# Optimization experiments

Measured on AMD Instinct MI355X. Metric: run time of the kernel, lower is better.

## Reference

```python
import jax, jax.numpy as jnp
import numpy as np

EMBED_DIM = 1024
N_HEADS = 16
HEAD_DIM = EMBED_DIM // N_HEADS


def setup_inputs() -> dict:
    key = jax.random.key(0)
    k1, k2, k3 = jax.random.split(key, 3)
    B, T, D = 2, 2048, EMBED_DIM
    x = jax.random.normal(k1, (B, T, D), dtype=jnp.float32)
    # torch nn.Linear weights: (out_features, in_features); y = x @ W.T
    scale = 1.0 / np.sqrt(D)
    qkv_w = jax.random.uniform(k2, (3 * D, D), dtype=jnp.float32, minval=-scale, maxval=scale)
    out_w = jax.random.uniform(k3, (D, D), dtype=jnp.float32, minval=-scale, maxval=scale)
    return {"x": x, "qkv_w": qkv_w, "out_w": out_w}


def reference(x, qkv_w, out_w):
    B, T, D = x.shape
    H, hd = N_HEADS, HEAD_DIM
    qkv = jnp.einsum('btd,ed->bte', x, qkv_w)  # (B,T,3D)
    qkv = qkv.reshape(B, T, 3, H, hd)
    q = jnp.transpose(qkv[:, :, 0], (0, 2, 1, 3))  # (B,H,T,hd)
    k = jnp.transpose(qkv[:, :, 1], (0, 2, 1, 3))
    v = jnp.transpose(qkv[:, :, 2], (0, 2, 1, 3))
    scores = jnp.einsum('bhtd,bhsd->bhts', q, k) / np.sqrt(hd).astype(np.float32)
    causal = jnp.tril(jnp.ones((T, T), dtype=bool))  # True = keep
    scores = jnp.where(causal[None, None], scores, -jnp.inf)
    probs = jax.nn.softmax(scores, axis=-1)
    out = jnp.einsum('bhts,bhsd->bhtd', probs, v)
    out = jnp.transpose(out, (0, 2, 1, 3)).reshape(B, T, D)
    return jnp.einsum('btd,ed->bte', out, out_w)
```

## Files before the change

### kernel.cpp

```cpp
#include <hip/hip_runtime.h>
#include <hip/hip_bf16.h>
#include <stdint.h>

typedef __bf16 bf16;
typedef __attribute__((ext_vector_type(8))) __bf16 bf16x8;
typedef __attribute__((ext_vector_type(4))) __bf16 bf16x4;
typedef __attribute__((ext_vector_type(4))) float f32x4;

#define AS1 __attribute__((address_space(1)))
#define AS3 __attribute__((address_space(3)))

__device__ __forceinline__ void async16(const void* g, void* l) {
  __builtin_amdgcn_global_load_lds((AS1 uint32_t*)(g), (AS3 uint32_t*)(l), 16, 0, 0);
}

__device__ __forceinline__ f32x4 mfma_bf16(bf16x8 a, bf16x8 b, f32x4 c) {
  return __builtin_amdgcn_mfma_f32_16x16x32_bf16(a, b, c, 0, 0, 0);
}

__device__ __forceinline__ uint32_t pack2_bf16(float a, float b) {
  union { __hip_bfloat162 h2; uint32_t u; } u;
  u.h2 = __float22bfloat162_rn(float2{a, b});
  return u.u;
}

__global__ __launch_bounds__(256) void cast_all_kernel(
    const float* __restrict__ x, const float* __restrict__ w1,
    const float* __restrict__ w2, bf16* __restrict__ xb,
    bf16* __restrict__ w1b, bf16* __restrict__ w2b) {
  const int bid = blockIdx.x;
  const float* src;
  bf16* dst;
  int base;
  if (bid < 4096) { src = x;  dst = xb;  base = bid; }
  else if (bid < 7168) { src = w1; dst = w1b; base = bid - 4096; }
  else { src = w2; dst = w2b; base = bid - 7168; }
  const int i = (base * 256 + threadIdx.x) * 4;
  const float4 v = *(const float4*)(src + i);
  bf16x4 o;
  o[0] = (bf16)v.x; o[1] = (bf16)v.y; o[2] = (bf16)v.z; o[3] = (bf16)v.w;
  *(bf16x4*)(dst + i) = o;
}

__global__ __launch_bounds__(256) void gemm_qkv_kernel(
    const bf16* __restrict__ A, const bf16* __restrict__ W,
    bf16* __restrict__ QK, bf16* __restrict__ VT) {
  constexpr int K = 1024;
  __shared__ __align__(16) bf16 sm[2 * 128 * 32];
  const int tid = threadIdx.x;
  const int w = tid >> 6, lane = tid & 63;
  const int m0 = blockIdx.x * 128, n0 = blockIdx.y * 128;
  const int wm = (w >> 1) * 64, wn = (w & 1) * 64;
  const int lrow = lane & 15, quad = lane >> 4;
  const int lk = quad * 8;
  f32x4 acc[4][4] = {};

  for (int k0 = 0; k0 < K; k0 += 32) {
#pragma unroll
    for (int i = 0; i < 4; ++i) {
      const int c = tid + 256 * i;
      const bf16* src = (c < 512)
          ? (A + (size_t)(m0 + (c >> 2)) * K + k0 + (c & 3) * 8)
          : (W + (size_t)(n0 + ((c - 512) >> 2)) * K + k0 + (c & 3) * 8);
      async16(src, sm + (w * 64 + i * 256) * 8);
    }
    __syncthreads();
    bf16x8 af[4], bfr[4];
#pragma unroll
    for (int mi = 0; mi < 4; ++mi)
      af[mi] = *(const bf16x8*)&sm[(wm + mi * 16 + lrow) * 32 + lk];
#pragma unroll
    for (int ni = 0; ni < 4; ++ni)
      bfr[ni] = *(const bf16x8*)&sm[128 * 32 + (wn + ni * 16 + lrow) * 32 + lk];
#pragma unroll
    for (int mi = 0; mi < 4; ++mi)
#pragma unroll
      for (int ni = 0; ni < 4; ++ni)
        acc[mi][ni] = mfma_bf16(af[mi], bfr[ni], acc[mi][ni]);
    __syncthreads();
  }

  bf16* s2 = sm;
  const bool isV = (n0 >= 2048);
  const int bb = m0 >> 11;
  const int mt = m0 & 2047;
  if (!isV) {
#pragma unroll
    for (int c = 0; c < 2; ++c) {
      if ((w >> 1) == c) {
#pragma unroll
        for (int mi = 0; mi < 4; ++mi)
#pragma unroll
          for (int ni = 0; ni < 4; ++ni) {
            const int nr = wn + ni * 16 + lrow;
#pragma unroll
            for (int r = 0; r < 4; ++r)
              s2[(mi * 16 + quad * 4 + r) * 128 + nr] = (bf16)acc[mi][ni][r];
          }
      }
      __syncthreads();
#pragma unroll
      for (int p = 0; p < 4; ++p) {
        const int row = p * 16 + (tid >> 4);
        const int colc = (tid & 15) * 8;
        const bf16x8 v = *(const bf16x8*)&s2[row * 128 + colc];
        *(bf16x8*)(QK + (size_t)(m0 + c * 64 + row) * 2048 + n0 + colc) = v;
      }
      __syncthreads();
    }
  } else {
#pragma unroll
    for (int c = 0; c < 2; ++c) {
      if ((w & 1) == c) {
#pragma unroll
        for (int mi = 0; mi < 4; ++mi)
#pragma unroll
          for (int ni = 0; ni < 4; ++ni) {
            const int nl = ni * 16 + lrow;
            bf16x4 pk4;
#pragma unroll
            for (int r = 0; r < 4; ++r) pk4[r] = (bf16)acc[mi][ni][r];
            *(bf16x4*)&s2[nl * 128 + wm + mi * 16 + quad * 4] = pk4;
          }
      }
      __syncthreads();
#pragma unroll
      for (int p = 0; p < 4; ++p) {
        const int row = p * 16 + (tid >> 4);
        const int colc = (tid & 15) * 8;
        const bf16x8 v = *(const bf16x8*)&s2[row * 128 + colc];
        const int vtrow = bb * 1024 + (n0 - 2048) + c * 64 + row;
        *(bf16x8*)(VT + (size_t)vtrow * 2048 + mt + colc) = v;
      }
      __syncthreads();
    }
  }
}

__global__ __launch_bounds__(512) void attn_kernel(
    const bf16* __restrict__ QK, const bf16* __restrict__ VT,
    bf16* __restrict__ AO) {
  __shared__ __align__(16) bf16 sK[2][2][64 * 64];
  __shared__ __align__(16) bf16 sV[2][2][64 * 64];
  const int bid = blockIdx.x;
  const int half = bid >> 8;
  const int i6 = bid & 255;
  const int bh = i6 & 31;
  const int g = half ? (i6 >> 5) : 15 - (i6 >> 5);
  const int b = bh >> 4, h = bh & 15;
  const int tid = threadIdx.x, w = tid >> 6, lane = tid & 63;
  const int qhalf = w >> 1, parity = w & 1;
  const int Q0 = g * 128;
  const int col = lane & 15, quad = lane >> 4;
  const bf16* Qb = QK + (size_t)b * 2048 * 2048 + h * 64;
  const bf16* Kb = Qb + 1024;
  const bf16* Vb = VT + (size_t)bh * 64 * 2048;
  const float NEG_INF = -__builtin_inff();
  constexpr float QSCALE = 0.18033688011112042f;

  union { uint32_t u[4]; bf16x8 v; } ones;
  ones.u[0] = 0x3F803F80u; ones.u[1] = 0x3F803F80u;
  ones.u[2] = 0x3F803F80u; ones.u[3] = 0x3F803F80u;

  int qrow[2];
  bf16x8 qf[2][2];
#pragma unroll
  for (int qtile = 0; qtile < 2; ++qtile) {
    qrow[qtile] = Q0 + qhalf * 32 + qtile * 16 + col;
#pragma unroll
    for (int kk = 0; kk < 2; ++kk) {
      bf16x8 v = *(const bf16x8*)(Qb + (size_t)qrow[qtile] * 2048 + kk * 32 + quad * 8);
#pragma unroll
      for (int e = 0; e < 8; ++e) v[e] = (bf16)((float)v[e] * QSCALE);
      qf[qtile][kk] = v;
    }
  }

  auto stage = [&](int s0, int cur) {
    bf16* dK = &sK[cur][0][0];
    bf16* dV = &sV[cur][0][0];
#pragma unroll
    for (int i = 0; i < 2; ++i) {
      const int L = tid + 512 * i;
      const int buf = L >> 9, Lr = L & 511;
      const int row = Lr >> 3;
      const int ch = (Lr & 7) ^ (row & 7);
      async16(Kb + (size_t)(s0 + buf * 64 + row) * 2048 + ch * 8, dK + L * 8);
    }
#pragma unroll
    for (int i = 0; i < 2; ++i) {
      const int L = tid + 512 * i;
      const int buf = L >> 9, Lr = L & 511;
      const int d = Lr >> 3;
      const int ch = (Lr & 7) ^ (d & 7);
      async16(Vb + (size_t)d * 2048 + s0 + buf * 64 + ch * 8, dV + L * 8);
    }
  };

  int srow[4];
#pragma unroll
  for (int m = 0; m < 4; ++m)
    srow[m] = 32 * (m & 1) + (col >> 2) * 8 + 4 * (m >> 1) + (col & 3);

  f32x4 accO[4][2] = {};
  f32x4 accL[2] = {};

  auto body = [&](int kv0, bool masked, int cur) {
    const bf16* kbuf = &sK[cur][parity][0];
    const bf16* vbuf = &sV[cur][parity][0];

    f32x4 st[2][4] = {};
#pragma unroll
    for (int kk = 0; kk < 2; ++kk) {
      bf16x8 kf[4];
#pragma unroll
      for (int m = 0; m < 4; ++m)
        kf[m] = *(const bf16x8*)&kbuf[srow[m] * 64 + (((kk * 4 + quad) ^ (srow[m] & 7)) * 8)];
      __builtin_amdgcn_s_setprio(1);
#pragma unroll
      for (int m = 0; m < 4; ++m)
#pragma unroll
        for (int qtile = 0; qtile < 2; ++qtile)
          st[qtile][m] = mfma_bf16(kf[m], qf[qtile][kk], st[qtile][m]);
      __builtin_amdgcn_s_setprio(0);
    }

    if (masked) {
#pragma unroll
      for (int qtile = 0; qtile < 2; ++qtile)
#pragma unroll
        for (int m = 0; m < 4; ++m) {
          const int kvb = kv0 + 32 * (m & 1) + quad * 8 + 4 * (m >> 1);
#pragma unroll
          for (int r = 0; r < 4; ++r)
            st[qtile][m][r] = (kvb + r <= qrow[qtile]) ? st[qtile][m][r] : NEG_INF;
        }
    }

    uint32_t pk[2][4][2];
#pragma unroll
    for (int qtile = 0; qtile < 2; ++qtile)
#pragma unroll
      for (int m = 0; m < 4; ++m) {
        const float p0 = __builtin_amdgcn_exp2f(st[qtile][m][0]);
        const float p1 = __builtin_amdgcn_exp2f(st[qtile][m][1]);
        const float p2 = __builtin_amdgcn_exp2f(st[qtile][m][2]);
        const float p3 = __builtin_amdgcn_exp2f(st[qtile][m][3]);
        pk[qtile][m][0] = pack2_bf16(p0, p1);
        pk[qtile][m][1] = pack2_bf16(p2, p3);
      }

#pragma unroll
    for (int kk = 0; kk < 2; ++kk) {
      bf16x8 vf[4];
#pragma unroll
      for (int d = 0; d < 4; ++d) {
        const int row = d * 16 + col;
        vf[d] = *(const bf16x8*)&vbuf[row * 64 + (((kk * 4 + quad) ^ (row & 7)) * 8)];
      }
      __builtin_amdgcn_s_setprio(1);
#pragma unroll
      for (int qtile = 0; qtile < 2; ++qtile) {
        union { uint32_t u[4]; bf16x8 v; } f;
        f.u[0] = pk[qtile][kk][0];
        f.u[1] = pk[qtile][kk][1];
        f.u[2] = pk[qtile][2 + kk][0];
        f.u[3] = pk[qtile][2 + kk][1];
        accL[qtile] = mfma_bf16(ones.v, f.v, accL[qtile]);
#pragma unroll
        for (int d = 0; d < 4; ++d)
          accO[d][qtile] = mfma_bf16(vf[d], f.v, accO[d][qtile]);
      }
      __builtin_amdgcn_s_setprio(0);
    }
  };

  const int npairs = g + 1;
  const int qmax = Q0 + qhalf * 32 + 31;
  stage(0, 0);
  int cur = 0;
  for (int j = 0; j < npairs; ++j) {
    if (j + 1 < npairs) {
      stage((j + 1) * 128, cur ^ 1);
      asm volatile("s_waitcnt vmcnt(4)" ::: "memory");
    } else {
      asm volatile("s_waitcnt vmcnt(0)" ::: "memory");
    }
    __builtin_amdgcn_s_barrier();
    const int kv0 = j * 128 + parity * 64;
    if (kv0 <= qmax)
      body(kv0, kv0 + 64 > Q0 + qhalf * 32, cur);
    __builtin_amdgcn_s_barrier();
    cur ^= 1;
  }

  float* scrO = (float*)sK;
  float* scrL = (float*)sV;
  if (parity == 1) {
    const int base = qhalf * 2048;
#pragma unroll
    for (int d = 0; d < 4; ++d)
#pragma unroll
      for (int qtile = 0; qtile < 2; ++qtile)
#pragma unroll
        for (int r = 0; r < 4; ++r)
          scrO[base + ((d * 2 + qtile) * 4 + r) * 64 + lane] = accO[d][qtile][r];
#pragma unroll
    for (int qtile = 0; qtile < 2; ++qtile)
      scrL[qhalf * 128 + qtile * 64 + lane] = accL[qtile][0];
  }
  __syncthreads();
  if (parity == 0) {
    const int base = qhalf * 2048;
#pragma unroll
    for (int d = 0; d < 4; ++d)
#pragma unroll
      for (int qtile = 0; qtile < 2; ++qtile)
#pragma unroll
        for (int r = 0; r < 4; ++r)
          accO[d][qtile][r] += scrO[base + ((d * 2 + qtile) * 4 + r) * 64 + lane];
    bf16* Ob = AO + (size_t)b * 2048 * 1024 + h * 64;
#pragma unroll
    for (int qtile = 0; qtile < 2; ++qtile) {
      const float inv = 1.0f / (accL[qtile][0] + scrL[qhalf * 128 + qtile * 64 + lane]);
#pragma unroll
      for (int d = 0; d < 4; ++d) {
        bf16x4 o;
#pragma unroll
        for (int r = 0; r < 4; ++r) o[r] = (bf16)(accO[d][qtile][r] * inv);
        *(bf16x4*)(Ob + (size_t)qrow[qtile] * 1024 + d * 16 + quad * 4) = o;
      }
    }
  }
}

__global__ __launch_bounds__(256) void gemm_out_kernel(
    const bf16* __restrict__ A, const bf16* __restrict__ W,
    float* __restrict__ C) {
  constexpr int K = 1024;
  __shared__ __align__(16) bf16 sm[2 * 128 * 32];
  const int tid = threadIdx.x;
  const int w = tid >> 6, lane = tid & 63;
  const int m0 = blockIdx.x * 128, n0 = blockIdx.y * 128;
  const int wm = (w >> 1) * 64, wn = (w & 1) * 64;
  const int lrow = lane & 15, lk = (lane >> 4) * 8;
  f32x4 acc[4][4] = {};

  for (int k0 = 0; k0 < K; k0 += 32) {
#pragma unroll
    for (int i = 0; i < 4; ++i) {
      const int c = tid + 256 * i;
      const bf16* src = (c < 512)
          ? (A + (size_t)(m0 + (c >> 2)) * K + k0 + (c & 3) * 8)
          : (W + (size_t)(n0 + ((c - 512) >> 2)) * K + k0 + (c & 3) * 8);
      async16(src, sm + (w * 64 + i * 256) * 8);
    }
    __syncthreads();
    bf16x8 af[4], bfr[4];
#pragma unroll
    for (int mi = 0; mi < 4; ++mi)
      af[mi] = *(const bf16x8*)&sm[(wm + mi * 16 + lrow) * 32 + lk];
#pragma unroll
    for (int ni = 0; ni < 4; ++ni)
      bfr[ni] = *(const bf16x8*)&sm[128 * 32 + (wn + ni * 16 + lrow) * 32 + lk];
#pragma unroll
    for (int mi = 0; mi < 4; ++mi)
#pragma unroll
      for (int ni = 0; ni < 4; ++ni)
        acc[mi][ni] = mfma_bf16(af[mi], bfr[ni], acc[mi][ni]);
    __syncthreads();
  }

#pragma unroll
  for (int mi = 0; mi < 4; ++mi)
#pragma unroll
    for (int ni = 0; ni < 4; ++ni) {
      const int n = n0 + wn + ni * 16 + lrow;
#pragma unroll
      for (int r = 0; r < 4; ++r) {
        const int m = m0 + wm + mi * 16 + (lane >> 4) * 4 + r;
        C[(size_t)m * 1024 + n] = acc[mi][ni][r];
      }
    }
}

extern "C" void kernel_launch(void* const* d_in, const int* in_sizes, int n_in,
                              void* d_out, int out_size, void* d_ws, size_t ws_size,
                              hipStream_t stream) {
  const float* x     = (const float*)d_in[0];
  const float* qkv_w = (const float*)d_in[1];
  const float* out_w = (const float*)d_in[2];
  float* out = (float*)d_out;

  char* ws = (char*)d_ws;
  bf16* xb    = (bf16*)(ws);
  bf16* aob   = (bf16*)(ws);
  bf16* wqkvb = (bf16*)(ws + 8u * 1024 * 1024);
  bf16* wob   = (bf16*)(ws + 14u * 1024 * 1024);
  bf16* qkb   = (bf16*)(ws + 16u * 1024 * 1024);
  bf16* vtb   = (bf16*)(ws + 32u * 1024 * 1024);

  cast_all_kernel<<<8192, 256, 0, stream>>>(x, qkv_w, out_w, xb, wqkvb, wob);
  gemm_qkv_kernel<<<dim3(32, 24), 256, 0, stream>>>(xb, wqkvb, qkb, vtb);
  attn_kernel<<<dim3(512), 512, 0, stream>>>(qkb, vtb, aob);
  gemm_out_kernel<<<dim3(32, 8), 256, 0, stream>>>(aob, wob, out);
}
```

Baseline: 175.6 us.

## Pair complementary causal query tiles per block and drop split-KV reduction

The attention kernel now launches 256 blocks, each handling two 128-row query tiles (tile 15-bp and tile bp), so every block does the same total of 17 KV pair-steps. Each wave owns 16 query rows and runs both 64-key halves of a staged 128-key chunk itself, instead of two waves splitting the KV range and merging partial sums through LDS. This removes the cross-wave reduction and the tail imbalance from causal masking. In exchange there is half as many blocks (256 vs 512, on a chip with 256 CUs), fewer independent MFMA chains per wave, and a longer serial loop per block.

```diff
diff --git a/kernel.cpp b/kernel.cpp
--- a/kernel.cpp
+++ b/kernel.cpp
@@ -143,37 +143,36 @@
   __shared__ __align__(16) bf16 sK[2][2][64 * 64];
   __shared__ __align__(16) bf16 sV[2][2][64 * 64];
   const int bid = blockIdx.x;
-  const int half = bid >> 8;
-  const int i6 = bid & 255;
-  const int bh = i6 & 31;
-  const int g = half ? (i6 >> 5) : 15 - (i6 >> 5);
+  const int bh = bid & 31;
+  const int bp = bid >> 5;
   const int b = bh >> 4, h = bh & 15;
   const int tid = threadIdx.x, w = tid >> 6, lane = tid & 63;
-  const int qhalf = w >> 1, parity = w & 1;
-  const int Q0 = g * 128;
   const int col = lane & 15, quad = lane >> 4;
   const bf16* Qb = QK + (size_t)b * 2048 * 2048 + h * 64;
   const bf16* Kb = Qb + 1024;
   const bf16* Vb = VT + (size_t)bh * 64 * 2048;
   const float NEG_INF = -__builtin_inff();
   constexpr float QSCALE = 0.18033688011112042f;
+  const int n0 = 16 - bp;
 
   union { uint32_t u[4]; bf16x8 v; } ones;
   ones.u[0] = 0x3F803F80u; ones.u[1] = 0x3F803F80u;
   ones.u[2] = 0x3F803F80u; ones.u[3] = 0x3F803F80u;
 
-  int qrow[2];
-  bf16x8 qf[2][2];
-#pragma unroll
-  for (int qtile = 0; qtile < 2; ++qtile) {
-    qrow[qtile] = Q0 + qhalf * 32 + qtile * 16 + col;
-#pragma unroll
-    for (int kk = 0; kk < 2; ++kk) {
-      bf16x8 v = *(const bf16x8*)(Qb + (size_t)qrow[qtile] * 2048 + kk * 32 + quad * 8);
-#pragma unroll
-      for (int e = 0; e < 8; ++e) v[e] = (bf16)((float)v[e] * QSCALE);
-      qf[qtile][kk] = v;
-    }
+  const int R0a = (15 - bp) * 128 + w * 16;
+  const int R0b = bp * 128 + w * 16;
+  const int qrow0 = R0a + col, qrow1 = R0b + col;
+  bf16x8 qf0[2], qf1[2];
+#pragma unroll
+  for (int kk = 0; kk < 2; ++kk) {
+    bf16x8 v0 = *(const bf16x8*)(Qb + (size_t)qrow0 * 2048 + kk * 32 + quad * 8);
+    bf16x8 v1 = *(const bf16x8*)(Qb + (size_t)qrow1 * 2048 + kk * 32 + quad * 8);
+#pragma unroll
+    for (int e = 0; e < 8; ++e) {
+      v0[e] = (bf16)((float)v0[e] * QSCALE);
+      v1[e] = (bf16)((float)v1[e] * QSCALE);
+    }
+    qf0[kk] = v0; qf1[kk] = v1;
   }
 
   auto stage = [&](int s0, int cur) {
@@ -202,14 +201,13 @@
   for (int m = 0; m < 4; ++m)
     srow[m] = 32 * (m & 1) + (col >> 2) * 8 + 4 * (m >> 1) + (col & 3);
 
-  f32x4 accO[4][2] = {};
-  f32x4 accL[2] = {};
-
-  auto body = [&](int kv0, bool masked, int cur) {
-    const bf16* kbuf = &sK[cur][parity][0];
-    const bf16* vbuf = &sV[cur][parity][0];
-
-    f32x4 st[2][4] = {};
+  f32x4 accO[4] = {};
+  f32x4 accL = {};
+
+  auto body = [&](const bf16* kbuf, const bf16* vbuf, bf16x8 qa, bf16x8 qb,
+                  int kv0, int qrowv, bool masked) {
+    f32x4 st[4] = {};
+    const bf16x8 qfl[2] = {qa, qb};
 #pragma unroll
     for (int kk = 0; kk < 2; ++kk) {
       bf16x8 kf[4];
@@ -219,36 +217,30 @@
       __builtin_amdgcn_s_setprio(1);
 #pragma unroll
       for (int m = 0; m < 4; ++m)
-#pragma unroll
-        for (int qtile = 0; qtile < 2; ++qtile)
-          st[qtile][m] = mfma_bf16(kf[m], qf[qtile][kk], st[qtile][m]);
+        st[m] = mfma_bf16(kf[m], qfl[kk], st[m]);
       __builtin_amdgcn_s_setprio(0);
     }
 
     if (masked) {
 #pragma unroll
-      for (int qtile = 0; qtile < 2; ++qtile)
-#pragma unroll
-        for (int m = 0; m < 4; ++m) {
-          const int kvb = kv0 + 32 * (m & 1) + quad * 8 + 4 * (m >> 1);
-#pragma unroll
-          for (int r = 0; r < 4; ++r)
-            st[qtile][m][r] = (kvb + r <= qrow[qtile]) ? st[qtile][m][r] : NEG_INF;
-        }
-    }
-
-    uint32_t pk[2][4][2];
-#pragma unroll
-    for (int qtile = 0; qtile < 2; ++qtile)
-#pragma unroll
       for (int m = 0; m < 4; ++m) {
-        const float p0 = __builtin_amdgcn_exp2f(st[qtile][m][0]);
-        const float p1 = __builtin_amdgcn_exp2f(st[qtile][m][1]);
-        const float p2 = __builtin_amdgcn_exp2f(st[qtile][m][2]);
-        const float p3 = __builtin_amdgcn_exp2f(st[qtile][m][3]);
-        pk[qtile][m][0] = pack2_bf16(p0, p1);
-        pk[qtile][m][1] = pack2_bf16(p2, p3);
-      }
+        const int kvb = kv0 + 32 * (m & 1) + quad * 8 + 4 * (m >> 1);
+#pragma unroll
+        for (int r = 0; r < 4; ++r)
+          st[m][r] = (kvb + r <= qrowv) ? st[m][r] : NEG_INF;
+      }
+    }
+
+    uint32_t pk[4][2];
+#pragma unroll
+    for (int m = 0; m < 4; ++m) {
+      const float p0 = __builtin_amdgcn_exp2f(st[m][0]);
+      const float p1 = __builtin_amdgcn_exp2f(st[m][1]);
+      const float p2 = __builtin_amdgcn_exp2f(st[m][2]);
+      const float p3 = __builtin_amdgcn_exp2f(st[m][3]);
+      pk[m][0] = pack2_bf16(p0, p1);
+      pk[m][1] = pack2_bf16(p2, p3);
+    }
 
 #pragma unroll
     for (int kk = 0; kk < 2; ++kk) {
@@ -258,80 +250,63 @@
         const int row = d * 16 + col;
         vf[d] = *(const bf16x8*)&vbuf[row * 64 + (((kk * 4 + quad) ^ (row & 7)) * 8)];
       }
+      union { uint32_t u[4]; bf16x8 v; } f;
+      f.u[0] = pk[kk][0];
+      f.u[1] = pk[kk][1];
+      f.u[2] = pk[2 + kk][0];
+      f.u[3] = pk[2 + kk][1];
       __builtin_amdgcn_s_setprio(1);
-#pragma unroll
-      for (int qtile = 0; qtile < 2; ++qtile) {
-        union { uint32_t u[4]; bf16x8 v; } f;
-        f.u[0] = pk[qtile][kk][0];
-        f.u[1] = pk[qtile][kk][1];
-        f.u[2] = pk[qtile][2 + kk][0];
-        f.u[3] = pk[qtile][2 + kk][1];
-        accL[qtile] = mfma_bf16(ones.v, f.v, accL[qtile]);
-#pragma unroll
-        for (int d = 0; d < 4; ++d)
-          accO[d][qtile] = mfma_bf16(vf[d], f.v, accO[d][qtile]);
-      }
+      accL = mfma_bf16(ones.v, f.v, accL);
+#pragma unroll
+      for (int d = 0; d < 4; ++d)
+        accO[d] = mfma_bf16(vf[d], f.v, accO[d]);
       __builtin_amdgcn_s_setprio(0);
     }
   };
 
-  const int npairs = g + 1;
-  const int qmax = Q0 + qhalf * 32 + 31;
+  auto runpair = [&](int j, int cur, bf16x8 qa, bf16x8 qb, int qrowv, int R0w) {
+    const int kv0 = j * 128;
+    if (kv0 <= R0w + 15)
+      body(&sK[cur][0][0], &sV[cur][0][0], qa, qb, kv0, qrowv, kv0 + 63 > R0w);
+    if (kv0 + 64 <= R0w + 15)
+      body(&sK[cur][1][0], &sV[cur][1][0], qa, qb, kv0 + 64, qrowv, kv0 + 127 > R0w);
+  };
+
+  auto writeout = [&](int qrowv) {
+    bf16* Ob = AO + (size_t)b * 2048 * 1024 + h * 64;
+    const float inv = 1.0f / accL[0];
+#pragma unroll
+    for (int d = 0; d < 4; ++d) {
+      bf16x4 o;
+#pragma unroll
+      for (int r = 0; r < 4; ++r) o[r] = (bf16)(accO[d][r] * inv);
+      *(bf16x4*)(Ob + (size_t)qrowv * 1024 + d * 16 + quad * 4) = o;
+    }
+  };
+
   stage(0, 0);
   int cur = 0;
-  for (int j = 0; j < npairs; ++j) {
-    if (j + 1 < npairs) {
-      stage((j + 1) * 128, cur ^ 1);
+  for (int i = 0; i < 17; ++i) {
+    if (i + 1 < 17) {
+      const int nx = (i + 1 < n0) ? (i + 1) : (i + 1 - n0);
+      stage(nx * 128, cur ^ 1);
       asm volatile("s_waitcnt vmcnt(4)" ::: "memory");
     } else {
       asm volatile("s_waitcnt vmcnt(0)" ::: "memory");
     }
     __builtin_amdgcn_s_barrier();
-    const int kv0 = j * 128 + parity * 64;
-    if (kv0 <= qmax)
-      body(kv0, kv0 + 64 > Q0 + qhalf * 32, cur);
+    if (i < n0) runpair(i, cur, qf0[0], qf0[1], qrow0, R0a);
+    else        runpair(i - n0, cur, qf1[0], qf1[1], qrow1, R0b);
+    if (i == n0 - 1) {
+      writeout(qrow0);
+#pragma unroll
+      for (int d = 0; d < 4; ++d) accO[d] = f32x4{0.f, 0.f, 0.f, 0.f};
+      accL = f32x4{0.f, 0.f, 0.f, 0.f};
+    }
     __builtin_amdgcn_s_barrier();
     cur ^= 1;
   }
-
-  float* scrO = (float*)sK;
-  float* scrL = (float*)sV;
-  if (parity == 1) {
-    const int base = qhalf * 2048;
-#pragma unroll
-    for (int d = 0; d < 4; ++d)
-#pragma unroll
-      for (int qtile = 0; qtile < 2; ++qtile)
-#pragma unroll
-        for (int r = 0; r < 4; ++r)
-          scrO[base + ((d * 2 + qtile) * 4 + r) * 64 + lane] = accO[d][qtile][r];
-#pragma unroll
-    for (int qtile = 0; qtile < 2; ++qtile)
-      scrL[qhalf * 128 + qtile * 64 + lane] = accL[qtile][0];
-  }
-  __syncthreads();
-  if (parity == 0) {
-    const int base = qhalf * 2048;
-#pragma unroll
-    for (int d = 0; d < 4; ++d)
-#pragma unroll
-      for (int qtile = 0; qtile < 2; ++qtile)
-#pragma unroll
-        for (int r = 0; r < 4; ++r)
-          accO[d][qtile][r] += scrO[base + ((d * 2 + qtile) * 4 + r) * 64 + lane];
-    bf16* Ob = AO + (size_t)b * 2048 * 1024 + h * 64;
-#pragma unroll
-    for (int qtile = 0; qtile < 2; ++qtile) {
-      const float inv = 1.0f / (accL[qtile][0] + scrL[qhalf * 128 + qtile * 64 + lane]);
-#pragma unroll
-      for (int d = 0; d < 4; ++d) {
-        bf16x4 o;
-#pragma unroll
-        for (int r = 0; r < 4; ++r) o[r] = (bf16)(accO[d][qtile][r] * inv);
-        *(bf16x4*)(Ob + (size_t)qrow[qtile] * 1024 + d * 16 + quad * 4) = o;
-      }
-    }
-  }
+  writeout(qrow1);
 }
 
 __global__ __launch_bounds__(256) void gemm_out_kernel(
@@ -402,6 +377,6 @@
 
   cast_all_kernel<<<8192, 256, 0, stream>>>(x, qkv_w, out_w, xb, wqkvb, wob);
   gemm_qkv_kernel<<<dim3(32, 24), 256, 0, stream>>>(xb, wqkvb, qkb, vtb);
-  attn_kernel<<<dim3(512), 512, 0, stream>>>(qkb, vtb, aob);
+  attn_kernel<<<dim3(256), 512, 0, stream>>>(qkb, vtb, aob);
   gemm_out_kernel<<<dim3(32, 8), 256, 0, stream>>>(aob, wob, out);
 }
```

New measurement: 172.5 us. Within noise of the previous version (-1.7%).
